# Kernel optimization log

Hardware: AMD Instinct MI355X
Metric: run time of the kernel (lower is better)

## Reference

```python
import jax, jax.numpy as jnp
import numpy as np

INPUT_SIZE = 1024
OUTPUT_SIZE = 15
EXPERT_NUM = 10
BS = 65536


def setup_inputs() -> dict:
    key = jax.random.key(0)
    k1, k2, k3, k4, k5 = jax.random.split(key, 5)
    bound = 1.0 / np.sqrt(INPUT_SIZE)
    x = jax.random.normal(k1, (BS, INPUT_SIZE), dtype=jnp.float32)
    expert_w = jax.random.uniform(k2, (EXPERT_NUM, OUTPUT_SIZE, INPUT_SIZE), minval=-bound, maxval=bound, dtype=jnp.float32)
    expert_b = jax.random.uniform(k3, (EXPERT_NUM, OUTPUT_SIZE), minval=-bound, maxval=bound, dtype=jnp.float32)
    gate_w = jax.random.uniform(k4, (EXPERT_NUM, OUTPUT_SIZE, INPUT_SIZE), minval=-bound, maxval=bound, dtype=jnp.float32)
    gate_b = jax.random.uniform(k5, (EXPERT_NUM, OUTPUT_SIZE), minval=-bound, maxval=bound, dtype=jnp.float32)
    return {"x": x, "expert_w": expert_w, "expert_b": expert_b, "gate_w": gate_w, "gate_b": gate_b}


def reference(x, expert_w, expert_b, gate_w, gate_b):
    # miu, xi: (bs, out, E) -- matches torch.stack(..., dim=-1)
    miu = jnp.einsum('bi,eoi->boe', x, expert_w) + expert_b.T[None]  # (bs, out, E)
    xi = jnp.einsum('bi,eoi->boe', x, gate_w) + gate_b.T[None]       # (bs, out, E)
    g = jax.nn.softmax(xi, axis=-1)                                  # softmax over experts
    return jnp.sum(g * miu, axis=-1)                                 # (bs, out)
```

## Files before the change

kernel.cpp:

```cpp
#include <hip/hip_runtime.h>

#define KDIM 1024
#define NOUT 15
#define NEXP 10
#define BM   64
#define NKS  32
#define QPT  20
#define SCOL 305
#define XSTR 36

typedef short bf16x8 __attribute__((ext_vector_type(8)));
typedef float f32x16 __attribute__((ext_vector_type(16)));

__device__ __forceinline__ unsigned f2bf2(float a, float b) {
    unsigned ua = __float_as_uint(a);
    unsigned ub = __float_as_uint(b);
    ua = (ua + 0x7FFFu + ((ua >> 16) & 1u)) >> 16;
    ub = (ub + 0x7FFFu + ((ub >> 16) & 1u)) & 0xFFFF0000u;
    return ua | ub;
}

__device__ __forceinline__ void dma16(const void* g, void* l) {
    __builtin_amdgcn_global_load_lds(
        (const __attribute__((address_space(1))) unsigned int*)g,
        (__attribute__((address_space(3))) unsigned int*)l, 16, 0, 0);
}

__global__ void wconv_kernel(const float* __restrict__ ew,
                             const float* __restrict__ gw,
                             unsigned short* __restrict__ ws)
{
    int U  = blockIdx.x * 256 + threadIdx.x;
    int L  = U & 63;
    int q  = (U >> 6) % QPT;
    int ks = U / (QPT * 64);
    int nt = q >> 1, kt = q & 1;
    int wrow = nt * 32 + (L & 31);
    int wcol = ks * 32 + kt * 16 + (L >> 5) * 8;
    float4 a = {0.f,0.f,0.f,0.f}, b = {0.f,0.f,0.f,0.f};
    if (wrow < 150) {
        a = *(const float4*)(ew + wrow * KDIM + wcol);
        b = *(const float4*)(ew + wrow * KDIM + wcol + 4);
    } else if (wrow < 300) {
        a = *(const float4*)(gw + (wrow - 150) * KDIM + wcol);
        b = *(const float4*)(gw + (wrow - 150) * KDIM + wcol + 4);
    }
    uint4 o;
    o.x = f2bf2(a.x, a.y); o.y = f2bf2(a.z, a.w);
    o.z = f2bf2(b.x, b.y); o.w = f2bf2(b.z, b.w);
    *(uint4*)(ws + (size_t)U * 8) = o;
}

__global__ void __launch_bounds__(256, 3)
moe_kernel(const float* __restrict__ x,
           const unsigned short* __restrict__ wsrc,
           const float* __restrict__ eb,
           const float* __restrict__ gb,
           float* __restrict__ out)
{
    __shared__ union {
        struct {
            unsigned short wb[2][QPT * 512];
            unsigned short xb[2][64 * XSTR];
        } k;
        float ep[32][SCOL];
    } sm;

    const int tid = threadIdx.x;
    const int wv  = tid >> 6;
    const int L   = tid & 63;
    const int mw  = wv >> 1;
    const int nw  = wv & 1;
    const int ln  = L & 31;
    const int lh  = L >> 5;

    const int srow = tid >> 2;
    const int schk = tid & 3;
    const float* xg = x + ((size_t)blockIdx.x * BM + srow) * KDIM + schk * 8;
    const int xwo = srow * XSTR + schk * 8;

    const int xfo = (mw * 32 + ln) * XSTR + lh * 8;

    f32x16 acc[5];
    #pragma unroll
    for (int nt = 0; nt < 5; ++nt)
        #pragma unroll
        for (int r = 0; r < 16; ++r)
            acc[nt][r] = 0.f;

    #pragma unroll
    for (int i = 0; i < 5; ++i) {
        int q = wv * 5 + i;
        dma16(wsrc + ((size_t)q * 64 + L) * 8, &sm.k.wb[0][q * 512]);
    }
    {
        float4 a = *(const float4*)(xg);
        float4 b = *(const float4*)(xg + 4);
        uint4 o;
        o.x = f2bf2(a.x, a.y); o.y = f2bf2(a.z, a.w);
        o.z = f2bf2(b.x, b.y); o.w = f2bf2(b.z, b.w);
        *(uint4*)&sm.k.xb[0][xwo] = o;
    }
    float4 xa0 = *(const float4*)(xg + 32);
    float4 xa1 = *(const float4*)(xg + 32 + 4);
    __syncthreads();

    #pragma unroll 2
    for (int ks = 0; ks < NKS; ++ks) {
        float4 xn0 = {0.f,0.f,0.f,0.f}, xn1 = {0.f,0.f,0.f,0.f};
        if (ks + 2 < NKS) {
            xn0 = *(const float4*)(xg + (ks + 2) * 32);
            xn1 = *(const float4*)(xg + (ks + 2) * 32 + 4);
        }
        if (ks + 1 < NKS) {
            #pragma unroll
            for (int i = 0; i < 5; ++i) {
                int q = wv * 5 + i;
                dma16(wsrc + (((size_t)(ks + 1) * QPT + q) * 64 + L) * 8,
                      &sm.k.wb[(ks + 1) & 1][q * 512]);
            }
            uint4 o;
            o.x = f2bf2(xa0.x, xa0.y); o.y = f2bf2(xa0.z, xa0.w);
            o.z = f2bf2(xa1.x, xa1.y); o.w = f2bf2(xa1.z, xa1.w);
            *(uint4*)&sm.k.xb[(ks + 1) & 1][xwo] = o;
        }

        const unsigned short* xbuf = sm.k.xb[ks & 1];
        bf16x8 af0 = *(const bf16x8*)&xbuf[xfo];
        bf16x8 af1 = *(const bf16x8*)&xbuf[xfo + 16];

        const unsigned short* wbuf = sm.k.wb[ks & 1];
        #pragma unroll
        for (int nt = 0; nt < 5; ++nt) {
            int q = (nw * 5 + nt) * 2;
            bf16x8 b0 = *(const bf16x8*)&wbuf[q * 512 + L * 8];
            bf16x8 b1 = *(const bf16x8*)&wbuf[(q + 1) * 512 + L * 8];
            acc[nt] = __builtin_amdgcn_mfma_f32_32x32x16_bf16(af0, b0, acc[nt], 0, 0, 0);
            acc[nt] = __builtin_amdgcn_mfma_f32_32x32x16_bf16(af1, b1, acc[nt], 0, 0, 0);
        }
        __syncthreads();

        xa0 = xn0;
        xa1 = xn1;
    }

    #pragma unroll 1
    for (int g = 0; g < 2; ++g) {
        if (mw == g) {
            #pragma unroll
            for (int nt = 0; nt < 5; ++nt) {
                int col = nw * 160 + nt * 32 + ln;
                if (col < 300) {
                    #pragma unroll
                    for (int r = 0; r < 16; ++r)
                        sm.ep[(r & 3) + 8 * (r >> 2) + 4 * lh][col] = acc[nt][r];
                }
            }
        }
        __syncthreads();

        #pragma unroll 1
        for (int t = tid; t < 32 * NOUT; t += 256) {
            int row = t / NOUT, o = t % NOUT;
            float xi[NEXP], miu_v[NEXP];
            float mx = -1e30f;
            #pragma unroll
            for (int e = 0; e < NEXP; ++e) {
                miu_v[e] = sm.ep[row][e * NOUT + o]       + eb[e * NOUT + o];
                xi[e]    = sm.ep[row][150 + e * NOUT + o] + gb[e * NOUT + o];
                mx = fmaxf(mx, xi[e]);
            }
            float s = 0.f, v = 0.f;
            #pragma unroll
            for (int e = 0; e < NEXP; ++e) {
                float g2 = __expf(xi[e] - mx);
                s += g2;
                v += g2 * miu_v[e];
            }
            out[((size_t)blockIdx.x * BM + g * 32 + row) * NOUT + o] = v / s;
        }
        __syncthreads();
    }
}

extern "C" void kernel_launch(void* const* d_in, const int* in_sizes, int n_in,
                              void* d_out, int out_size, void* d_ws, size_t ws_size,
                              hipStream_t stream) {
    const float* x  = (const float*)d_in[0];
    const float* ew = (const float*)d_in[1];
    const float* eb = (const float*)d_in[2];
    const float* gw = (const float*)d_in[3];
    const float* gb = (const float*)d_in[4];
    float* out = (float*)d_out;
    unsigned short* ws = (unsigned short*)d_ws;

    wconv_kernel<<<160, 256, 0, stream>>>(ew, gw, ws);
    moe_kernel<<<65536 / BM, 256, 0, stream>>>(x, ws, eb, gb, out);
}
```

Baseline: 456.1 us.

## Hand-pipeline K loop with partial vmcnt barriers and pad x tile stride

Unrolls the K loop by two with explicit ping-pong buffers. Plain __syncthreads is replaced by barriers that wait only until two loads remain outstanding, so the prefetched x global loads stay in flight across the barrier while the weight DMA into LDS must complete. sched_barrier fences pin the order of issue, conversion and MFMA work. The x LDS row stride changes from 36 to 40 halves, making rows 16-byte aligned for the vector LDS reads and writes. The hand-written waitcnt depends on in-order counting of the five DMA loads and two x loads, which is brittle if the compiler reorders or adds memory operations.

```diff
diff --git a/kernel.cpp b/kernel.cpp
--- a/kernel.cpp
+++ b/kernel.cpp
@@ -7,7 +7,7 @@
 #define NKS  32
 #define QPT  20
 #define SCOL 305
-#define XSTR 36
+#define XSTR 40
 
 typedef short bf16x8 __attribute__((ext_vector_type(8)));
 typedef float f32x16 __attribute__((ext_vector_type(16)));
@@ -24,6 +24,43 @@
     __builtin_amdgcn_global_load_lds(
         (const __attribute__((address_space(1))) unsigned int*)g,
         (__attribute__((address_space(3))) unsigned int*)l, 16, 0, 0);
+}
+
+__device__ __forceinline__ void kbar2() {
+    __builtin_amdgcn_sched_barrier(0);
+    asm volatile("s_waitcnt vmcnt(2) lgkmcnt(0)" ::: "memory");
+    __builtin_amdgcn_s_barrier();
+    __builtin_amdgcn_sched_barrier(0);
+}
+__device__ __forceinline__ void kbar0() {
+    __builtin_amdgcn_sched_barrier(0);
+    asm volatile("s_waitcnt vmcnt(0) lgkmcnt(0)" ::: "memory");
+    __builtin_amdgcn_s_barrier();
+    __builtin_amdgcn_sched_barrier(0);
+}
+
+__device__ __forceinline__ void xwrite(unsigned short* xs, int xwo, const float4 (&v)[2]) {
+    uint4 o;
+    o.x = f2bf2(v[0].x, v[0].y); o.y = f2bf2(v[0].z, v[0].w);
+    o.z = f2bf2(v[1].x, v[1].y); o.w = f2bf2(v[1].z, v[1].w);
+    *(uint4*)&xs[xwo] = o;
+}
+
+__device__ __forceinline__ void compute_slab(const unsigned short* wbuf,
+                                             const unsigned short* xbuf,
+                                             int xfo, int nw, int L,
+                                             f32x16 (&acc)[5])
+{
+    bf16x8 af0 = *(const bf16x8*)&xbuf[xfo];
+    bf16x8 af1 = *(const bf16x8*)&xbuf[xfo + 16];
+    #pragma unroll
+    for (int nt = 0; nt < 5; ++nt) {
+        int q = (nw * 5 + nt) * 2;
+        bf16x8 b0 = *(const bf16x8*)&wbuf[q * 512 + L * 8];
+        bf16x8 b1 = *(const bf16x8*)&wbuf[(q + 1) * 512 + L * 8];
+        acc[nt] = __builtin_amdgcn_mfma_f32_32x32x16_bf16(af0, b0, acc[nt], 0, 0, 0);
+        acc[nt] = __builtin_amdgcn_mfma_f32_32x32x16_bf16(af1, b1, acc[nt], 0, 0, 0);
+    }
 }
 
 __global__ void wconv_kernel(const float* __restrict__ ew,
@@ -61,7 +98,7 @@
     __shared__ union {
         struct {
             unsigned short wb[2][QPT * 512];
-            unsigned short xb[2][64 * XSTR];
+            unsigned short xs[2][64 * XSTR];
         } k;
         float ep[32][SCOL];
     } sm;
@@ -74,11 +111,8 @@
     const int ln  = L & 31;
     const int lh  = L >> 5;
 
-    const int srow = tid >> 2;
-    const int schk = tid & 3;
-    const float* xg = x + ((size_t)blockIdx.x * BM + srow) * KDIM + schk * 8;
-    const int xwo = srow * XSTR + schk * 8;
-
+    const float* xg = x + ((size_t)blockIdx.x * BM + (tid >> 2)) * KDIM + (tid & 3) * 8;
+    const int xwo = (tid >> 2) * XSTR + (tid & 3) * 8;
     const int xfo = (mw * 32 + ln) * XSTR + lh * 8;
 
     f32x16 acc[5];
@@ -87,61 +121,70 @@
         #pragma unroll
         for (int r = 0; r < 16; ++r)
             acc[nt][r] = 0.f;
+
+    float4 xa[2], xb[2];
 
     #pragma unroll
     for (int i = 0; i < 5; ++i) {
         int q = wv * 5 + i;
         dma16(wsrc + ((size_t)q * 64 + L) * 8, &sm.k.wb[0][q * 512]);
     }
+    __builtin_amdgcn_sched_barrier(0);
     {
-        float4 a = *(const float4*)(xg);
-        float4 b = *(const float4*)(xg + 4);
-        uint4 o;
-        o.x = f2bf2(a.x, a.y); o.y = f2bf2(a.z, a.w);
-        o.z = f2bf2(b.x, b.y); o.w = f2bf2(b.z, b.w);
-        *(uint4*)&sm.k.xb[0][xwo] = o;
-    }
-    float4 xa0 = *(const float4*)(xg + 32);
-    float4 xa1 = *(const float4*)(xg + 32 + 4);
-    __syncthreads();
-
-    #pragma unroll 2
-    for (int ks = 0; ks < NKS; ++ks) {
-        float4 xn0 = {0.f,0.f,0.f,0.f}, xn1 = {0.f,0.f,0.f,0.f};
-        if (ks + 2 < NKS) {
-            xn0 = *(const float4*)(xg + (ks + 2) * 32);
-            xn1 = *(const float4*)(xg + (ks + 2) * 32 + 4);
-        }
-        if (ks + 1 < NKS) {
-            #pragma unroll
-            for (int i = 0; i < 5; ++i) {
-                int q = wv * 5 + i;
-                dma16(wsrc + (((size_t)(ks + 1) * QPT + q) * 64 + L) * 8,
-                      &sm.k.wb[(ks + 1) & 1][q * 512]);
-            }
-            uint4 o;
-            o.x = f2bf2(xa0.x, xa0.y); o.y = f2bf2(xa0.z, xa0.w);
-            o.z = f2bf2(xa1.x, xa1.y); o.w = f2bf2(xa1.z, xa1.w);
-            *(uint4*)&sm.k.xb[(ks + 1) & 1][xwo] = o;
-        }
-
-        const unsigned short* xbuf = sm.k.xb[ks & 1];
-        bf16x8 af0 = *(const bf16x8*)&xbuf[xfo];
-        bf16x8 af1 = *(const bf16x8*)&xbuf[xfo + 16];
-
-        const unsigned short* wbuf = sm.k.wb[ks & 1];
-        #pragma unroll
-        for (int nt = 0; nt < 5; ++nt) {
-            int q = (nw * 5 + nt) * 2;
-            bf16x8 b0 = *(const bf16x8*)&wbuf[q * 512 + L * 8];
-            bf16x8 b1 = *(const bf16x8*)&wbuf[(q + 1) * 512 + L * 8];
-            acc[nt] = __builtin_amdgcn_mfma_f32_32x32x16_bf16(af0, b0, acc[nt], 0, 0, 0);
-            acc[nt] = __builtin_amdgcn_mfma_f32_32x32x16_bf16(af1, b1, acc[nt], 0, 0, 0);
-        }
+        float4 xt[2];
+        xt[0] = *(const float4*)(xg);
+        xt[1] = *(const float4*)(xg + 4);
+        __builtin_amdgcn_sched_barrier(0);
+        xa[0] = *(const float4*)(xg + 32);
+        xa[1] = *(const float4*)(xg + 32 + 4);
+        __builtin_amdgcn_sched_barrier(0);
+        xwrite(sm.k.xs[0], xwo, xt);
+    }
+    kbar2();
+
+    #pragma unroll 1
+    for (int s = 0; s < 30; s += 2) {
+        #pragma unroll
+        for (int i = 0; i < 5; ++i) {
+            int q = wv * 5 + i;
+            dma16(wsrc + (((size_t)(s + 1) * QPT + q) * 64 + L) * 8,
+                  &sm.k.wb[(s + 1) & 1][q * 512]);
+        }
+        __builtin_amdgcn_sched_barrier(0);
+        xb[0] = *(const float4*)(xg + (s + 2) * 32);
+        xb[1] = *(const float4*)(xg + (s + 2) * 32 + 4);
+        __builtin_amdgcn_sched_barrier(0);
+        xwrite(sm.k.xs[(s + 1) & 1], xwo, xa);
+        compute_slab(sm.k.wb[s & 1], sm.k.xs[s & 1], xfo, nw, L, acc);
+        kbar2();
+
+        #pragma unroll
+        for (int i = 0; i < 5; ++i) {
+            int q = wv * 5 + i;
+            dma16(wsrc + (((size_t)(s + 2) * QPT + q) * 64 + L) * 8,
+                  &sm.k.wb[s & 1][q * 512]);
+        }
+        __builtin_amdgcn_sched_barrier(0);
+        xa[0] = *(const float4*)(xg + (s + 3) * 32);
+        xa[1] = *(const float4*)(xg + (s + 3) * 32 + 4);
+        __builtin_amdgcn_sched_barrier(0);
+        xwrite(sm.k.xs[s & 1], xwo, xb);
+        compute_slab(sm.k.wb[(s + 1) & 1], sm.k.xs[(s + 1) & 1], xfo, nw, L, acc);
+        kbar2();
+    }
+
+    {
+        #pragma unroll
+        for (int i = 0; i < 5; ++i) {
+            int q = wv * 5 + i;
+            dma16(wsrc + (((size_t)31 * QPT + q) * 64 + L) * 8, &sm.k.wb[1][q * 512]);
+        }
+        __builtin_amdgcn_sched_barrier(0);
+        xwrite(sm.k.xs[1], xwo, xa);
+        compute_slab(sm.k.wb[0], sm.k.xs[0], xfo, nw, L, acc);
+        kbar0();
+        compute_slab(sm.k.wb[1], sm.k.xs[1], xfo, nw, L, acc);
         __syncthreads();
-
-        xa0 = xn0;
-        xa1 = xn1;
     }
 
     #pragma unroll 1
```

Result: faster. 397.7 us (-12.8%).
